# Kernel optimization log

Hardware: AMD Instinct MI355X
Metric: run time of the kernel (lower is better)

Reference implementation:

```python
import jax, jax.numpy as jnp
import numpy as np

BATCH, LENGTH, DIM = 2, 2048, 1024
DIM_HIDDEN, NUM_HEAD = 1024, 8
BASE_LR, BASE_WD = 0.01, 0.01


def setup_inputs() -> dict:
    key = jax.random.key(0)
    ks = jax.random.split(key, 8)
    s = jnp.float32(0.02)  # init scale for linear weights
    f32 = jnp.float32
    return {
        "x": jax.random.normal(ks[0], (BATCH, LENGTH, DIM), f32),
        "hidden": jax.random.normal(ks[1], (BATCH, DIM, DIM_HIDDEN), f32),
        "log_base_lr": jnp.full((NUM_HEAD,), float(np.log(BASE_LR)), f32),
        "fc_lr_w": jax.random.normal(ks[2], (DIM, NUM_HEAD), f32) * s,
        "fc_lr_b": jnp.zeros((NUM_HEAD,), f32),
        "log_base_wd": jnp.full((NUM_HEAD,), float(np.log(BASE_WD)), f32),
        "fc_wd_w": jax.random.normal(ks[3], (DIM, NUM_HEAD), f32) * s,
        "fc_wd_b": jnp.zeros((NUM_HEAD,), f32),
        "wq": jax.random.normal(ks[4], (DIM, DIM_HIDDEN), f32) * s,
        "bq": jnp.zeros((DIM_HIDDEN,), f32),
        "wk": jax.random.normal(ks[5], (DIM, DIM_HIDDEN), f32) * s,
        "bk": jnp.zeros((DIM_HIDDEN,), f32),
        "wv": jax.random.normal(ks[6], (DIM, DIM), f32) * s,
        "bv": jnp.zeros((DIM,), f32),
    }


def reference(x, hidden, log_base_lr, fc_lr_w, fc_lr_b, log_base_wd, fc_wd_w, fc_wd_b, wq, bq, wk, bk, wv, bv):
    b, L, dim = x.shape
    n = log_base_lr.shape[0]
    dim_hidden = wq.shape[1]
    dh = dim_hidden // n

    W_prev = hidden.reshape(b, dim, n, dh).transpose(0, 2, 1, 3)          # [b,n,dim,h]
    q = (x @ wq + bq).reshape(b, L, n, dh).transpose(0, 2, 1, 3)          # [b,n,L,h]
    k = (x @ wk + bk).reshape(b, L, n, dh).transpose(0, 2, 1, 3)          # [b,n,L,h]
    v = x @ wv + bv                                                        # [b,L,dim]

    lr = (jnp.exp(log_base_lr) * jax.nn.sigmoid(x @ fc_lr_w + fc_lr_b)).transpose(0, 2, 1)   # [b,n,L]
    lwd = jnp.log1p(-jnp.exp(log_base_wd) * jax.nn.sigmoid(x @ fc_wd_w + fc_wd_b)).transpose(0, 2, 1)  # [b,n,L]

    wd_cross = jnp.exp(jnp.cumsum(lwd, axis=2))                            # [b,n,L]
    # einops.repeat 'b n l -> b n m l' then triu(1), cumsum over m, exp, triu
    rep = jnp.broadcast_to(lwd[:, :, None, :], (b, n, L, L))               # [b,n,m,l]
    wd_inner = jnp.triu(jnp.exp(jnp.cumsum(jnp.triu(rep, 1), axis=2)))     # [b,n,L,L]

    kq = jnp.einsum('bnld,bnmd->bnlm', k, q)                               # [b,n,L,L]
    mask_kq = kq * wd_inner

    WpK_V = jnp.einsum('bndh,bnlh->bnld', W_prev, k) - v[:, None]          # [b,n,L,dim]

    y_inner = -jnp.einsum('bnld,bnl,bnlm->bmd', WpK_V, lr, mask_kq)        # [b,L,dim]
    y_cross = jnp.einsum('bndh,bnlh,bnl->bld', W_prev, q, wd_cross)        # [b,L,dim]
    y = y_inner + y_cross

    Wn_inner = -jnp.einsum('bnld,bnl,bnlh->bndh', WpK_V, lr * wd_inner[:, :, :, -1], k)
    Wn_cross = W_prev * wd_cross[:, :, -1][:, :, None, None]
    W_next = (Wn_inner + Wn_cross).transpose(0, 2, 1, 3).reshape(b, dim, dim_hidden)
    return (y, W_next)
```

## Files before the change

kernel.cpp:

```cpp
#include <hip/hip_runtime.h>
#include <stdint.h>


typedef __bf16 bf16x8 __attribute__((ext_vector_type(8)));
typedef float f32x4 __attribute__((ext_vector_type(4)));
typedef unsigned short u16;
typedef u16 u16x4 __attribute__((ext_vector_type(4)));

#define MFMA16 __builtin_amdgcn_mfma_f32_16x16x32_bf16

static __device__ __forceinline__ u16 f2b(float f) {
  union { float f; uint32_t u; } v; v.f = f;
  uint32_t r = v.u + 0x7FFFu + ((v.u >> 16) & 1u);
  return (u16)(r >> 16);
}
static __device__ __forceinline__ float b2f(u16 h) {
  union { uint32_t u; float f; } v; v.u = ((uint32_t)h) << 16;
  return v.f;
}

typedef __attribute__((address_space(1))) void gvoid_t;
typedef __attribute__((address_space(3))) void lvoid_t;
static __device__ __forceinline__ void gld16(const u16* g, u16* l) {
  __builtin_amdgcn_global_load_lds((gvoid_t*)(uintptr_t)g, (lvoid_t*)l, 16, 0, 0);
}
static __device__ __forceinline__ void stage(u16* lds, const u16* __restrict__ g, int ld, int t) {
  const int r0 = t >> 2, c0 = (t & 3) << 3;
  gld16(g + (size_t)r0 * ld + c0, lds + (r0 << 5) + c0);
  gld16(g + (size_t)(r0 + 64) * ld + c0, lds + ((r0 + 64) << 5) + c0);
}

#define TILE_IDS                                   \
  const int t = threadIdx.x;                       \
  const int w = t >> 6, ln = t & 63;               \
  const int wr = (w >> 1) << 6, wc = (w & 1) << 6; \
  const int q = ln >> 4, q8 = q << 3, r = ln & 15;

static __device__ __forceinline__ void mfma_tile(const u16* As, const u16* Bs,
                                                 int wr, int wc, int q8, int r, f32x4 acc[4][4]) {
  bf16x8 af[4], bf[4];
#pragma unroll
  for (int s = 0; s < 4; ++s) af[s] = *(const bf16x8*)(As + ((wr + s * 16 + r) << 5) + q8);
#pragma unroll
  for (int s = 0; s < 4; ++s) bf[s] = *(const bf16x8*)(Bs + ((wc + s * 16 + r) << 5) + q8);
#pragma unroll
  for (int sm = 0; sm < 4; ++sm)
#pragma unroll
    for (int sn = 0; sn < 4; ++sn)
      acc[sm][sn] = MFMA16(af[sm], bf[sn], acc[sm][sn], 0, 0, 0);
}


__global__ __launch_bounds__(256) void k_cast(const float* __restrict__ s, u16* __restrict__ d) {
  const size_t i = ((size_t)blockIdx.x * 256 + threadIdx.x) * 4;
  f32x4 v = *(const f32x4*)(s + i);
  u16x4 o;
#pragma unroll
  for (int j = 0; j < 4; ++j) o[j] = f2b(v[j]);
  *(u16x4*)(d + i) = o;
}

__global__ __launch_bounds__(256) void k_zero(float* __restrict__ p) {
  const size_t i = ((size_t)blockIdx.x * 256 + threadIdx.x) * 4;
  *(f32x4*)(p + i) = f32x4{0.f, 0.f, 0.f, 0.f};
}

__global__ __launch_bounds__(256) void k_twt(const float* __restrict__ wq, const float* __restrict__ wk,
                                             const float* __restrict__ wv, u16* __restrict__ wqT,
                                             u16* __restrict__ wkT, u16* __restrict__ wvT) {
  const int z = blockIdx.z;
  const float* src = z == 0 ? wq : z == 1 ? wk : wv;
  u16* dst = z == 0 ? wqT : z == 1 ? wkT : wvT;
  __shared__ float tile[32][33];
  const int k0 = blockIdx.x * 32, n0 = blockIdx.y * 32;
  const int tx = threadIdx.x, ty = threadIdx.y;
#pragma unroll
  for (int i = 0; i < 4; ++i)
    tile[ty + i * 8][tx] = src[(size_t)(k0 + ty + i * 8) * 1024 + n0 + tx];
  __syncthreads();
#pragma unroll
  for (int i = 0; i < 4; ++i)
    dst[(size_t)(n0 + ty + i * 8) * 1024 + k0 + tx] = f2b(tile[tx][ty + i * 8]);
}

__global__ __launch_bounds__(256) void k_lrwd(const float* __restrict__ x,
    const float* __restrict__ wlr, const float* __restrict__ blr,
    const float* __restrict__ wwd, const float* __restrict__ bwd,
    const float* __restrict__ lbl, const float* __restrict__ lbw,
    float* __restrict__ lr, float* __restrict__ lwd) {
  const int row = blockIdx.x;
  const int t = threadIdx.x;
  float pl[8] = {}, pw[8] = {};
  const float* xr = x + (size_t)row * 1024;
  for (int i = t; i < 1024; i += 256) {
    const float xv = xr[i];
    const float* wl = wlr + (size_t)i * 8;
    const float* ww = wwd + (size_t)i * 8;
#pragma unroll
    for (int j = 0; j < 8; ++j) { pl[j] += xv * wl[j]; pw[j] += xv * ww[j]; }
  }
  __shared__ float red[256][17];
#pragma unroll
  for (int j = 0; j < 8; ++j) { red[t][j] = pl[j]; red[t][j + 8] = pw[j]; }
  __syncthreads();
  for (int s = 128; s > 0; s >>= 1) {
    if (t < s) {
#pragma unroll
      for (int j = 0; j < 16; ++j) red[t][j] += red[t + s][j];
    }
    __syncthreads();
  }
  const int b = row >> 11, l = row & 2047;
  if (t < 8) {
    const float sig = 1.f / (1.f + expf(-(red[0][t] + blr[t])));
    lr[((size_t)b * 8 + t) * 2048 + l] = expf(lbl[t]) * sig;
  } else if (t < 16) {
    const int j = t - 8;
    const float sig = 1.f / (1.f + expf(-(red[0][t] + bwd[j])));
    lwd[((size_t)b * 8 + j) * 2048 + l] = log1pf(-expf(lbw[j]) * sig);
  }
}

__global__ __launch_bounds__(256) void k_scan(const float* __restrict__ lwd,
                                              float* __restrict__ wdc, float* __restrict__ wdlast) {
  const int bn = blockIdx.x, t = threadIdx.x;
  const float* src = lwd + (size_t)bn * 2048;
  float v[8], s = 0.f;
#pragma unroll
  for (int i = 0; i < 8; ++i) { v[i] = src[t * 8 + i]; s += v[i]; }
  __shared__ float ps[256];
  ps[t] = s;
  __syncthreads();
  for (int off = 1; off < 256; off <<= 1) {
    const float add = (t >= off) ? ps[t - off] : 0.f;
    __syncthreads();
    ps[t] += add;
    __syncthreads();
  }
  float run = ps[t] - s;
  const float lwd_last = src[2047];
  float* wo = wdc + (size_t)bn * 2048;
  float* wl = wdlast + (size_t)bn * 2048;
#pragma unroll
  for (int i = 0; i < 8; ++i) {
    run += v[i];
    const int idx = t * 8 + i;
    wo[idx] = expf(run);
    const int c = (idx + 1 < 2047) ? (idx + 1) : 2047;
    wl[idx] = expf(lwd_last * (float)c);
  }
}

__global__ __launch_bounds__(256) void k_qs(u16* __restrict__ qb, const float* __restrict__ wdc) {
  const size_t base = ((size_t)blockIdx.x * 256 + threadIdx.x) * 4;
  const int b = (int)(base >> 21);
  const int rem = (int)(base & 2097151);
  const int m = rem >> 10, hd = rem & 1023;
  const float sc = wdc[((size_t)b * 8 + (hd >> 7)) * 2048 + m];
  u16x4 v = *(const u16x4*)(qb + base);
#pragma unroll
  for (int j = 0; j < 4; ++j) v[j] = f2b(b2f(v[j]) * sc);
  *(u16x4*)(qb + base) = v;
}


__global__ __launch_bounds__(256) void g_qk(const u16* __restrict__ xb, const u16* __restrict__ wqT,
    const u16* __restrict__ wkT, const float* __restrict__ bq, const float* __restrict__ bk,
    u16* __restrict__ qb, u16* __restrict__ kb) {
  __shared__ u16 As[4096], Bs[4096];
  TILE_IDS
  const int m0 = blockIdx.x * 128, n0 = blockIdx.y * 128, z = blockIdx.z;
  const u16* A = xb + (size_t)m0 * 1024;
  const u16* B = (z ? wkT : wqT) + (size_t)n0 * 1024;
  const float* bias = z ? bk : bq;
  u16* outp = z ? kb : qb;
  f32x4 acc[4][4] = {};
  for (int k0 = 0; k0 < 1024; k0 += 32) {
    __syncthreads();
    stage(As, A + k0, 1024, t);
    stage(Bs, B + k0, 1024, t);
    __syncthreads();
    mfma_tile(As, Bs, wr, wc, q8, r, acc);
  }
#pragma unroll
  for (int sn = 0; sn < 4; ++sn) {
    const int col = n0 + wc + sn * 16 + r;
    const float bc = bias[col];
#pragma unroll
    for (int sm = 0; sm < 4; ++sm)
#pragma unroll
      for (int i = 0; i < 4; ++i) {
        const int gm = m0 + wr + sm * 16 + (q << 2) + i;
        outp[(size_t)gm * 1024 + col] = f2b(acc[sm][sn][i] + bc);
      }
  }
}

__global__ __launch_bounds__(256) void g_vtkt(const u16* __restrict__ xb, const u16* __restrict__ wvT,
    const u16* __restrict__ wkT, const float* __restrict__ bv, const float* __restrict__ bk,
    const float* __restrict__ wdl, u16* __restrict__ vT, u16* __restrict__ kTw) {
  __shared__ u16 As[4096], Bs[4096];
  TILE_IDS
  const int m0 = blockIdx.x * 128, l0 = blockIdx.y * 128;
  const int sel = blockIdx.z >> 1, b = blockIdx.z & 1;
  const u16* A = (sel ? wkT : wvT) + (size_t)m0 * 1024;
  const u16* B = xb + ((size_t)(b * 2048 + l0)) * 1024;
  f32x4 acc[4][4] = {};
  for (int k0 = 0; k0 < 1024; k0 += 32) {
    __syncthreads();
    stage(As, A + k0, 1024, t);
    stage(Bs, B + k0, 1024, t);
    __syncthreads();
    mfma_tile(As, Bs, wr, wc, q8, r, acc);
  }
#pragma unroll
  for (int sm = 0; sm < 4; ++sm)
#pragma unroll
    for (int i = 0; i < 4; ++i) {
      const int row = m0 + wr + sm * 16 + (q << 2) + i;
      const float bc = sel ? bk[row] : bv[row];
#pragma unroll
      for (int sn = 0; sn < 4; ++sn) {
        const int l = l0 + wc + sn * 16 + r;
        const float v = acc[sm][sn][i] + bc;
        if (!sel) {
          vT[((size_t)(b * 1024 + row)) * 2048 + l] = f2b(v);
        } else {
          const int n = row >> 7;
          kTw[((size_t)(b * 1024 + row)) * 2048 + l] =
              f2b(v * wdl[((size_t)(b * 8 + n)) * 2048 + l]);
        }
      }
    }
}

__global__ __launch_bounds__(256) void g2_s(const u16* __restrict__ qb, const u16* __restrict__ kb,
                                            const float* __restrict__ lwd, u16* __restrict__ S) {
  const int p = blockIdx.x, bn = blockIdx.y, b = bn >> 3, n = bn & 7;
  int mi = (int)((sqrtf(8.f * p + 1.f) - 1.f) * 0.5f);
  while ((mi + 1) * (mi + 2) / 2 <= p) ++mi;
  while (mi * (mi + 1) / 2 > p) --mi;
  const int li = p - mi * (mi + 1) / 2;
  const int m0 = mi * 128, l0 = li * 128;
  __shared__ u16 As[4096], Bs[4096];
  TILE_IDS
  const u16* A = qb + ((size_t)(b * 2048 + m0)) * 1024 + n * 128;
  const u16* B = kb + ((size_t)(b * 2048 + l0)) * 1024 + n * 128;
  f32x4 acc[4][4] = {};
  for (int k0 = 0; k0 < 128; k0 += 32) {
    __syncthreads();
    stage(As, A + k0, 1024, t);
    stage(Bs, B + k0, 1024, t);
    __syncthreads();
    mfma_tile(As, Bs, wr, wc, q8, r, acc);
  }
  const float* lwdp = lwd + (size_t)bn * 2048;
  u16* Sp = S + (size_t)bn * 2048 * 2048;
#pragma unroll
  for (int sm = 0; sm < 4; ++sm)
#pragma unroll
    for (int i = 0; i < 4; ++i) {
      const int m = m0 + wr + sm * 16 + (q << 2) + i;
      const float lm = lwdp[m];
#pragma unroll
      for (int sn = 0; sn < 4; ++sn) {
        const int l = l0 + wc + sn * 16 + r;
        float v = 0.f;
        if (l <= m) {
          const float c = (l == m) ? (float)m : (float)(l + 1);
          v = -acc[sm][sn][i] * __expf(lm * c);
        }
        Sp[(size_t)m * 2048 + l] = f2b(v);
      }
    }
}

__global__ __launch_bounds__(256) void g3_af(const u16* __restrict__ hb, const u16* __restrict__ kb,
                                             const u16* __restrict__ vT, const float* __restrict__ lr,
                                             u16* __restrict__ AfT) {
  const int d0 = blockIdx.x * 128, l0 = blockIdx.y * 128;
  const int bn = blockIdx.z, b = bn >> 3, n = bn & 7;
  __shared__ u16 As[4096], Bs[4096];
  TILE_IDS
  const u16* A = hb + ((size_t)(b * 1024 + d0)) * 1024 + n * 128;
  const u16* B = kb + ((size_t)(b * 2048 + l0)) * 1024 + n * 128;
  f32x4 acc[4][4] = {};
  for (int k0 = 0; k0 < 128; k0 += 32) {
    __syncthreads();
    stage(As, A + k0, 1024, t);
    stage(Bs, B + k0, 1024, t);
    __syncthreads();
    mfma_tile(As, Bs, wr, wc, q8, r, acc);
  }
  const float* lrp = lr + (size_t)bn * 2048;
#pragma unroll
  for (int sm = 0; sm < 4; ++sm)
#pragma unroll
    for (int i = 0; i < 4; ++i) {
      const int d = d0 + wr + sm * 16 + (q << 2) + i;
#pragma unroll
      for (int sn = 0; sn < 4; ++sn) {
        const int l = l0 + wc + sn * 16 + r;
        const float v = (acc[sm][sn][i] - b2f(vT[((size_t)(b * 1024 + d)) * 2048 + l])) * lrp[l];
        AfT[((size_t)bn * 1024 + d) * 2048 + l] = f2b(v);
      }
    }
}

__global__ __launch_bounds__(256) void g4(const u16* __restrict__ S, const u16* __restrict__ AfT,
                                          const u16* __restrict__ Qs, const u16* __restrict__ hb,
                                          float* __restrict__ y) {
  TILE_IDS
  const int mip = blockIdx.x, dj = blockIdx.y, z = blockIdx.z;
  const int b = z >> 1, half = z & 1;
  const int d0 = dj * 128;
  __shared__ u16 As[4096], Bs[4096];
  float* Y = y + (size_t)b * 2048 * 1024;
#pragma unroll 1
  for (int tsel = 0; tsel < 2; ++tsel) {
    const int mi = tsel ? (15 - mip) : mip;
    const int m0 = mi * 128;
    f32x4 acc[4][4] = {};
    for (int nh = 0; nh < 4; ++nh) {
      const int bn = b * 8 + half * 4 + nh;
      const u16* A = S + (size_t)bn * 2048 * 2048 + (size_t)m0 * 2048;
      const u16* B = AfT + ((size_t)bn * 1024 + d0) * 2048;
      const int nk = 4 * mi + 4;
      for (int c = 0; c < nk; ++c) {
        const int k0 = c * 32;
        __syncthreads();
        stage(As, A + k0, 2048, t);
        stage(Bs, B + k0, 2048, t);
        __syncthreads();
        mfma_tile(As, Bs, wr, wc, q8, r, acc);
      }
    }
    const u16* A2 = Qs + ((size_t)(b * 2048 + m0)) * 1024 + half * 512;
    const u16* B2 = hb + ((size_t)(b * 1024 + d0)) * 1024 + half * 512;
    for (int c = 0; c < 16; ++c) {
      const int k0 = c * 32;
      __syncthreads();
      stage(As, A2 + k0, 1024, t);
      stage(Bs, B2 + k0, 1024, t);
      __syncthreads();
      mfma_tile(As, Bs, wr, wc, q8, r, acc);
    }
#pragma unroll
    for (int sm = 0; sm < 4; ++sm)
#pragma unroll
      for (int i = 0; i < 4; ++i) {
        const int m = m0 + wr + sm * 16 + (q << 2) + i;
#pragma unroll
        for (int sn = 0; sn < 4; ++sn)
          atomicAdd(&Y[(size_t)m * 1024 + d0 + wc + sn * 16 + r], acc[sm][sn][i]);
      }
  }
}

__global__ __launch_bounds__(256) void g5_wn(const u16* __restrict__ AfT, const u16* __restrict__ kTw,
                                             const float* __restrict__ wdc, const float* __restrict__ hidden,
                                             float* __restrict__ outw) {
  const int d0 = blockIdx.x * 128, nj = blockIdx.y, b = blockIdx.z;
  const int bn = b * 8 + nj;
  __shared__ u16 As[4096], Bs[4096];
  TILE_IDS
  const u16* A = AfT + ((size_t)bn * 1024 + d0) * 2048;
  const u16* B = kTw + ((size_t)(b * 1024 + nj * 128)) * 2048;
  f32x4 acc[4][4] = {};
  for (int k0 = 0; k0 < 2048; k0 += 32) {
    __syncthreads();
    stage(As, A + k0, 2048, t);
    stage(Bs, B + k0, 2048, t);
    __syncthreads();
    mfma_tile(As, Bs, wr, wc, q8, r, acc);
  }
  const float wdcl = wdc[(size_t)bn * 2048 + 2047];
#pragma unroll
  for (int sm = 0; sm < 4; ++sm)
#pragma unroll
    for (int i = 0; i < 4; ++i) {
      const int d = d0 + wr + sm * 16 + (q << 2) + i;
#pragma unroll
      for (int sn = 0; sn < 4; ++sn) {
        const int hd = nj * 128 + wc + sn * 16 + r;
        const size_t off = ((size_t)(b * 1024 + d)) * 1024 + hd;
        outw[off] = hidden[off] * wdcl - acc[sm][sn][i];
      }
    }
}


extern "C" void kernel_launch(void* const* d_in, const int* in_sizes, int n_in,
                              void* d_out, int out_size, void* d_ws, size_t ws_size,
                              hipStream_t stream) {
  const float* x      = (const float*)d_in[0];
  const float* hidden = (const float*)d_in[1];
  const float* lbl    = (const float*)d_in[2];
  const float* wlr    = (const float*)d_in[3];
  const float* blr    = (const float*)d_in[4];
  const float* lbw    = (const float*)d_in[5];
  const float* wwd    = (const float*)d_in[6];
  const float* bwd    = (const float*)d_in[7];
  const float* wq     = (const float*)d_in[8];
  const float* bq     = (const float*)d_in[9];
  const float* wk     = (const float*)d_in[10];
  const float* bk     = (const float*)d_in[11];
  const float* wv     = (const float*)d_in[12];
  const float* bv     = (const float*)d_in[13];
  float* out = (float*)d_out;

  char* ws = (char*)d_ws;
  const size_t MB = 1u << 20;
  u16* S     = (u16*)(ws);
  u16* xb    = (u16*)(ws);
  u16* wqT   = (u16*)(ws + 8 * MB);
  u16* wkT   = (u16*)(ws + 10 * MB);
  u16* wvT   = (u16*)(ws + 12 * MB);
  u16* AfT   = (u16*)(ws + 128 * MB);
  u16* hb    = (u16*)(ws + 192 * MB);
  u16* qb    = (u16*)(ws + 196 * MB);
  u16* kb    = (u16*)(ws + 204 * MB);
  u16* kTw   = (u16*)(ws + 212 * MB);
  u16* vT    = (u16*)(ws + 220 * MB);
  float* lr  = (float*)(ws + 228 * MB);
  float* lwd = (float*)(ws + 228 * MB + 131072);
  float* wdc = (float*)(ws + 228 * MB + 262144);
  float* wdl = (float*)(ws + 228 * MB + 393216);
  (void)ws_size; (void)n_in; (void)in_sizes; (void)out_size;

  const size_t YSZ = (size_t)2 * 2048 * 1024;

  k_cast<<<4096, 256, 0, stream>>>(x, xb);
  k_cast<<<2048, 256, 0, stream>>>(hidden, hb);
  k_twt<<<dim3(32, 32, 3), dim3(32, 8), 0, stream>>>(wq, wk, wv, wqT, wkT, wvT);
  k_lrwd<<<4096, 256, 0, stream>>>(x, wlr, blr, wwd, bwd, lbl, lbw, lr, lwd);
  k_scan<<<16, 256, 0, stream>>>(lwd, wdc, wdl);
  g_qk<<<dim3(32, 8, 2), 256, 0, stream>>>(xb, wqT, wkT, bq, bk, qb, kb);
  g_vtkt<<<dim3(8, 16, 4), 256, 0, stream>>>(xb, wvT, wkT, bv, bk, wdl, vT, kTw);
  g2_s<<<dim3(136, 16), 256, 0, stream>>>(qb, kb, lwd, S);
  k_qs<<<4096, 256, 0, stream>>>(qb, wdc);
  g3_af<<<dim3(8, 16, 16), 256, 0, stream>>>(hb, kb, vT, lr, AfT);
  k_zero<<<4096, 256, 0, stream>>>(out);
  g4<<<dim3(8, 8, 4), 256, 0, stream>>>(S, AfT, qb, hb, out);
  g5_wn<<<dim3(8, 8, 2), 256, 0, stream>>>(AfT, kTw, wdc, hidden, out + YSZ);
}
```

Measured before the change: 504.6 us.

## Split g4 per head and g5 along K, reducing partial results with atomics

g4 now launches one block per head instead of per half of the heads, which gives four times as many blocks and a shorter serial K loop in each. g5_wn splits its 2048-long K reduction into four chunks and accumulates them with atomicAdd into an output that a new kernel, k_wninit, first fills with hidden scaled by the decay. Both changes raise parallelism on a grid that was too small for the GPU. The cost is more atomic traffic, an extra pass to initialise the output, and summation order that varies between runs.

```diff
diff --git a/kernel.cpp b/kernel.cpp
--- a/kernel.cpp
+++ b/kernel.cpp
@@ -63,6 +63,18 @@
 __global__ __launch_bounds__(256) void k_zero(float* __restrict__ p) {
   const size_t i = ((size_t)blockIdx.x * 256 + threadIdx.x) * 4;
   *(f32x4*)(p + i) = f32x4{0.f, 0.f, 0.f, 0.f};
+}
+
+__global__ __launch_bounds__(256) void k_wninit(const float* __restrict__ hidden,
+                                                const float* __restrict__ wdc,
+                                                float* __restrict__ out2) {
+  const size_t i = ((size_t)blockIdx.x * 256 + threadIdx.x) * 4;
+  const int b = (int)(i >> 20);
+  const int hd = (int)(i & 1023);
+  const float wdcl = wdc[((size_t)(b * 8 + (hd >> 7))) * 2048 + 2047];
+  f32x4 v = *(const f32x4*)(hidden + i);
+  v *= wdcl;
+  *(f32x4*)(out2 + i) = v;
 }
 
 __global__ __launch_bounds__(256) void k_twt(const float* __restrict__ wq, const float* __restrict__ wk,
@@ -312,7 +324,7 @@
                                           float* __restrict__ y) {
   TILE_IDS
   const int mip = blockIdx.x, dj = blockIdx.y, z = blockIdx.z;
-  const int b = z >> 1, half = z & 1;
+  const int b = z >> 3, n = z & 7;
   const int d0 = dj * 128;
   __shared__ u16 As[4096], Bs[4096];
   float* Y = y + (size_t)b * 2048 * 1024;
@@ -321,23 +333,20 @@
     const int mi = tsel ? (15 - mip) : mip;
     const int m0 = mi * 128;
     f32x4 acc[4][4] = {};
-    for (int nh = 0; nh < 4; ++nh) {
-      const int bn = b * 8 + half * 4 + nh;
-      const u16* A = S + (size_t)bn * 2048 * 2048 + (size_t)m0 * 2048;
-      const u16* B = AfT + ((size_t)bn * 1024 + d0) * 2048;
-      const int nk = 4 * mi + 4;
-      for (int c = 0; c < nk; ++c) {
-        const int k0 = c * 32;
-        __syncthreads();
-        stage(As, A + k0, 2048, t);
-        stage(Bs, B + k0, 2048, t);
-        __syncthreads();
-        mfma_tile(As, Bs, wr, wc, q8, r, acc);
-      }
-    }
-    const u16* A2 = Qs + ((size_t)(b * 2048 + m0)) * 1024 + half * 512;
-    const u16* B2 = hb + ((size_t)(b * 1024 + d0)) * 1024 + half * 512;
-    for (int c = 0; c < 16; ++c) {
+    const u16* A = S + (size_t)z * 2048 * 2048 + (size_t)m0 * 2048;
+    const u16* B = AfT + ((size_t)z * 1024 + d0) * 2048;
+    const int nk = 4 * mi + 4;
+    for (int c = 0; c < nk; ++c) {
+      const int k0 = c * 32;
+      __syncthreads();
+      stage(As, A + k0, 2048, t);
+      stage(Bs, B + k0, 2048, t);
+      __syncthreads();
+      mfma_tile(As, Bs, wr, wc, q8, r, acc);
+    }
+    const u16* A2 = Qs + ((size_t)(b * 2048 + m0)) * 1024 + n * 128;
+    const u16* B2 = hb + ((size_t)(b * 1024 + d0)) * 1024 + n * 128;
+    for (int c = 0; c < 4; ++c) {
       const int k0 = c * 32;
       __syncthreads();
       stage(As, A2 + k0, 1024, t);
@@ -358,23 +367,22 @@
 }
 
 __global__ __launch_bounds__(256) void g5_wn(const u16* __restrict__ AfT, const u16* __restrict__ kTw,
-                                             const float* __restrict__ wdc, const float* __restrict__ hidden,
-                                             float* __restrict__ outw) {
-  const int d0 = blockIdx.x * 128, nj = blockIdx.y, b = blockIdx.z;
+                                             float* __restrict__ out2) {
+  const int d0 = blockIdx.x * 128, nj = blockIdx.y;
+  const int z = blockIdx.z, b = z >> 2, kc = z & 3;
   const int bn = b * 8 + nj;
   __shared__ u16 As[4096], Bs[4096];
   TILE_IDS
-  const u16* A = AfT + ((size_t)bn * 1024 + d0) * 2048;
-  const u16* B = kTw + ((size_t)(b * 1024 + nj * 128)) * 2048;
+  const u16* A = AfT + ((size_t)bn * 1024 + d0) * 2048 + kc * 512;
+  const u16* B = kTw + ((size_t)(b * 1024 + nj * 128)) * 2048 + kc * 512;
   f32x4 acc[4][4] = {};
-  for (int k0 = 0; k0 < 2048; k0 += 32) {
+  for (int k0 = 0; k0 < 512; k0 += 32) {
     __syncthreads();
     stage(As, A + k0, 2048, t);
     stage(Bs, B + k0, 2048, t);
     __syncthreads();
     mfma_tile(As, Bs, wr, wc, q8, r, acc);
   }
-  const float wdcl = wdc[(size_t)bn * 2048 + 2047];
 #pragma unroll
   for (int sm = 0; sm < 4; ++sm)
 #pragma unroll
@@ -383,8 +391,7 @@
 #pragma unroll
       for (int sn = 0; sn < 4; ++sn) {
         const int hd = nj * 128 + wc + sn * 16 + r;
-        const size_t off = ((size_t)(b * 1024 + d)) * 1024 + hd;
-        outw[off] = hidden[off] * wdcl - acc[sm][sn][i];
+        atomicAdd(&out2[((size_t)(b * 1024 + d)) * 1024 + hd], -acc[sm][sn][i]);
       }
     }
 }
@@ -441,6 +448,7 @@
   k_qs<<<4096, 256, 0, stream>>>(qb, wdc);
   g3_af<<<dim3(8, 16, 16), 256, 0, stream>>>(hb, kb, vT, lr, AfT);
   k_zero<<<4096, 256, 0, stream>>>(out);
-  g4<<<dim3(8, 8, 4), 256, 0, stream>>>(S, AfT, qb, hb, out);
-  g5_wn<<<dim3(8, 8, 2), 256, 0, stream>>>(AfT, kTw, wdc, hidden, out + YSZ);
-}
+  k_wninit<<<2048, 256, 0, stream>>>(hidden, wdc, out + YSZ);
+  g4<<<dim3(8, 8, 16), 256, 0, stream>>>(S, AfT, qb, hb, out);
+  g5_wn<<<dim3(8, 8, 8), 256, 0, stream>>>(AfT, kTw, out + YSZ);
+}
```

Result: no change. 506.9 us (+0.4%).
